# Kernel tuning notes

Hardware: AMD Instinct MI355X
Metric: run time of the kernel (lower is better)

Reference implementation:

```python
import jax, jax.numpy as jnp
import numpy as np

H, N, L = 512, 64, 2048


def setup_inputs() -> dict:
    key = jax.random.key(0)
    ks = jax.random.split(key, 9)
    x = jax.random.normal(ks[0], (L, H), jnp.float32)
    # HiPPO-style diagonal-plus-low-rank init (stable: Re(Lambda) < 0)
    lambda_re = -0.5 * jnp.ones((N,), jnp.float32)
    lambda_im = jnp.pi * jnp.arange(N, dtype=jnp.float32)
    p_re = jax.random.normal(ks[1], (N,), jnp.float32) / np.sqrt(2 * N)
    p_im = jax.random.normal(ks[2], (N,), jnp.float32) / np.sqrt(2 * N)
    b_re = jax.random.normal(ks[3], (N,), jnp.float32)
    b_im = jax.random.normal(ks[4], (N,), jnp.float32)
    c_re = jax.random.normal(ks[5], (N,), jnp.float32)
    c_im = jax.random.normal(ks[6], (N,), jnp.float32)
    log_step = jnp.array(np.log(0.01), jnp.float32)
    w1 = jax.random.normal(ks[7], (H, H), jnp.float32) / np.sqrt(H)
    bias1 = jnp.zeros((H,), jnp.float32)
    w2 = jax.random.normal(ks[8], (H, H), jnp.float32) / np.sqrt(H)
    bias2 = jnp.zeros((H,), jnp.float32)
    return dict(x=x, lambda_re=lambda_re, lambda_im=lambda_im, p_re=p_re, p_im=p_im,
                b_re=b_re, b_im=b_im, c_re=c_re, c_im=c_im, log_step=log_step,
                w1=w1, bias1=bias1, w2=w2, bias2=bias2)


def _discrete_dplr(Lam, P, B, C, step, seq_len):
    # Bilinear discretization of the DPLR SSM A = diag(Lam) - P P^* (annotated-S4).
    n = Lam.shape[0]
    I = jnp.eye(n, dtype=jnp.complex64)
    A = jnp.diag(Lam) - P[:, None] * jnp.conj(P)[None, :]
    A0 = (2.0 / step) * I + A
    Dd = jnp.diag(1.0 / (2.0 / step - Lam))  # (2/dt - Lam)^{-1} diagonal
    Qc = jnp.conj(P)[None, :]                 # (1, N)
    P2 = P[:, None]                           # (N, 1)
    A1 = Dd - (Dd @ P2) @ (Qc @ Dd) / (1.0 + (Qc @ Dd @ P2))  # Woodbury
    Ab = A1 @ A0                               # (N, N) discrete transition
    Bb = 2.0 * (A1 @ B[:, None])[:, 0]         # (N,)
    Cb = jnp.conj(
        C[None, :] @ jnp.conj(jnp.linalg.inv(I - jnp.linalg.matrix_power(Ab, seq_len)))
    )[0]                                       # (N,)
    return Ab, Bb, Cb


def reference(x, lambda_re, lambda_im, p_re, p_im, b_re, b_im, c_re, c_im,
              log_step, w1, bias1, w2, bias2):
    seq_len, hidden = x.shape
    Lam = (lambda_re + 1j * lambda_im).astype(jnp.complex64)
    P = (p_re + 1j * p_im).astype(jnp.complex64)
    B = (b_re + 1j * b_im).astype(jnp.complex64)
    C = (c_re + 1j * c_im).astype(jnp.complex64)
    step = jnp.exp(log_step)
    Ab, Bb, Cb = _discrete_dplr(Lam, P, B, C, step, seq_len)

    skip = x
    state0 = jnp.zeros((hidden, Lam.shape[0]), jnp.complex64)  # (H, N)

    def step_fn(state, u_l):  # u_l: (H,) real inputs at one timestep
        state = state @ Ab.T + u_l[:, None] * Bb[None, :]  # (H, N)
        y = (state @ Cb).real                               # (H,)
        return state, y

    _, ys = jax.lax.scan(step_fn, state0, x)  # ys: (L, H)
    h = jax.nn.gelu(ys)
    out = (h @ w1.T + bias1) * jax.nn.sigmoid(h @ w2.T + bias2)
    return skip + out
```

## Files before the change

### kernel.cpp

```cpp
#include <hip/hip_runtime.h>
#include <hip/hip_bf16.h>

typedef unsigned short u16;
typedef short s16x8 __attribute__((ext_vector_type(8)));
typedef u16 u16x8 __attribute__((ext_vector_type(8)));
typedef unsigned int u32x4 __attribute__((ext_vector_type(4)));
typedef float f32x4 __attribute__((ext_vector_type(4)));

struct cplx { float x, y; };

#define L_SEQ 2048
#define HID 512
#define NST 64

__device__ __align__(16) cplx g_khat[L_SEQ];
__device__ __align__(16) float g_k[L_SEQ];
__device__ __align__(16) u16 g_Td[32 * 64 * 64];
__device__ __align__(16) u16 g_Xt[HID * L_SEQ];
__device__ __align__(16) u16 g_W1[HID * HID];
__device__ __align__(16) u16 g_W2[HID * HID];
__device__ __align__(16) u16 g_H[L_SEQ * HID];

__device__ __forceinline__ u16 f2bf(float f) {
    union { __hip_bfloat16 h; u16 u; } cv;
    cv.h = __float2bfloat16(f);
    return cv.u;
}

__global__ __launch_bounds__(256) void fused_convert(
    const float* x, const float* w1, const float* w2,
    const float* lre, const float* lim, const float* pre, const float* pim,
    const float* bre, const float* bim, const float* cre, const float* cim,
    const float* lstep) {
    __shared__ float tile[64][65];
    __shared__ float sLre[NST], sLim[NST], sPre[NST], sPim[NST];
    __shared__ float sBre[NST], sBim[NST], sCre[NST], sCim[NST];
    int b = blockIdx.x, tid = threadIdx.x;
    if (b < 256) {
        int lt = b >> 3, ht = b & 7;
#pragma unroll
        for (int i = 0; i < 4; i++) {
            int idx = i * 256 + tid;
            int r = idx >> 4, c4 = idx & 15;
            f32x4 v = *(const f32x4*)&x[(lt * 64 + r) * HID + ht * 64 + c4 * 4];
            tile[r][c4 * 4 + 0] = v.x;
            tile[r][c4 * 4 + 1] = v.y;
            tile[r][c4 * 4 + 2] = v.z;
            tile[r][c4 * 4 + 3] = v.w;
        }
        __syncthreads();
#pragma unroll
        for (int i = 0; i < 2; i++) {
            int idx = i * 256 + tid;
            int rr = idx >> 3, c8 = idx & 7;
            u16x8 v;
#pragma unroll
            for (int q = 0; q < 8; q++) v[q] = f2bf(tile[c8 * 8 + q][rr]);
            *(u16x8*)&g_Xt[(ht * 64 + rr) * L_SEQ + lt * 64 + c8 * 8] = v;
        }
    } else if (b < 768) {
        int t = (b - 256) * 256 + tid;
        const float* src = (t < 65536) ? w1 : w2;
        u16* dst = (t < 65536) ? g_W1 : g_W2;
        int idx = (t < 65536) ? t : (t - 65536);
        float4 v = ((const float4*)src)[idx];
        unsigned long long pk = (unsigned long long)f2bf(v.x) |
                                ((unsigned long long)f2bf(v.y) << 16) |
                                ((unsigned long long)f2bf(v.z) << 32) |
                                ((unsigned long long)f2bf(v.w) << 48);
        ((unsigned long long*)dst)[idx] = pk;
    } else {
        if (tid < NST) {
            sLre[tid] = lre[tid]; sLim[tid] = lim[tid];
            sPre[tid] = pre[tid]; sPim[tid] = pim[tid];
            sBre[tid] = bre[tid]; sBim[tid] = bim[tid];
            sCre[tid] = cre[tid]; sCim[tid] = cim[tid];
        }
        __syncthreads();
        int j = (b - 768) * 256 + tid;
        float tdt = 2.0f * __expf(-lstep[0]);
        float th = 0.00306796157577128245f * j;
        float sn, cs;
        __sincosf(th, &sn, &cs);
        float aRe = tdt * (1.f - cs), aIm = tdt * sn;
        float bRe = 1.f + cs, bIm = -sn;
        float cBx = 0.f, cBy = 0.f, cPx = 0.f, cPy = 0.f;
        float pBx = 0.f, pBy = 0.f, pPx = 0.f, pPy = 0.f;
#pragma unroll 8
        for (int n = 0; n < NST; n++) {
            float Lre = sLre[n], Lim = sLim[n];
            float Dre = aRe - (bRe * Lre - bIm * Lim);
            float Dim = aIm - (bRe * Lim + bIm * Lre);
            float inv = 1.f / (Dre * Dre + Dim * Dim);
            float eRe = Dre * inv, eIm = -Dim * inv;
            float cRe = sCre[n], cIm = -sCim[n];
            float t1Re = cRe * eRe - cIm * eIm, t1Im = cRe * eIm + cIm * eRe;
            float qRe = sPre[n], qIm = -sPim[n];
            float t2Re = qRe * eRe - qIm * eIm, t2Im = qRe * eIm + qIm * eRe;
            float BRe = sBre[n], BIm = sBim[n], PRe = sPre[n], PIm = sPim[n];
            cBx += t1Re * BRe - t1Im * BIm; cBy += t1Re * BIm + t1Im * BRe;
            cPx += t1Re * PRe - t1Im * PIm; cPy += t1Re * PIm + t1Im * PRe;
            pBx += t2Re * BRe - t2Im * BIm; pBy += t2Re * BIm + t2Im * BRe;
            pPx += t2Re * PRe - t2Im * PIm; pPy += t2Re * PIm + t2Im * PRe;
        }
        float denx = 1.f + (bRe * pPx - bIm * pPy);
        float deny = (bRe * pPy + bIm * pPx);
        float bcPx = bRe * cPx - bIm * cPy;
        float bcPy = bRe * cPy + bIm * cPx;
        float numx = bcPx * pBx - bcPy * pBy;
        float numy = bcPx * pBy + bcPy * pBx;
        float dinv = 1.f / (denx * denx + deny * deny);
        float corx = (numx * denx + numy * deny) * dinv;
        float cory = (numy * denx - numx * deny) * dinv;
        g_khat[j] = { 2.f * (cBx - corx), 2.f * (cBy - cory) };
    }
}

__global__ __launch_bounds__(256) void k_ifft() {
    int tid = threadIdx.x;
    int l = tid & 63;
    int t = blockIdx.x * 4 + (tid >> 6);
    float acc = 0.f;
#pragma unroll
    for (int i = 0; i < 16; i++) {
        int j = l + 64 * i;
        cplx a = g_khat[j];
        cplx b = g_khat[(2048 - j) & 2047];
        float re = 0.5f * (a.x + b.x);
        float im = 0.5f * (a.y - b.y);
        int idx = (j * t) & 2047;
        float s, c;
        __sincosf(0.00306796157577128245f * idx, &s, &c);
        float wgt = (j == 0) ? 1.f : 2.f;
        acc += wgt * (re * c - im * s);
    }
    if (l == 0) acc += (1 - 2 * (t & 1)) * g_khat[1024].x;
#pragma unroll
    for (int off = 1; off < 64; off <<= 1) acc += __shfl_xor(acc, off);
    if (l == 0) g_k[t] = acc * (1.f / 2048.f);
}

__global__ __launch_bounds__(256) void build_Td() {
    int gid = blockIdx.x * 256 + threadIdx.x;
    int o = gid * 8;
    int d = o >> 12, rem = o & 4095;
    int r = rem >> 6, c0 = rem & 63;
    int base = d * 64 + r - c0;
    u16x8 v;
#pragma unroll
    for (int q = 0; q < 8; q++) {
        int idx = base - q;
        v[q] = (idx >= 0) ? f2bf(g_k[idx]) : (u16)0;
    }
    *(u16x8*)&g_Td[o] = v;
}

__global__ __launch_bounds__(256) void conv_gemm() {
    __shared__ __align__(16) u16 As[64 * 128];
    __shared__ __align__(16) u16 Bs[64 * 128];
    int tid = threadIdx.x, l = tid & 63, w = tid >> 6;
    int wm = w >> 1, wn = w & 1;
    int bm = blockIdx.x >> 3, bn = blockIdx.x & 7;
    f32x4 acc[2][2] = {};
    int nst = (bm >> 1) + 1;
    int row0 = tid >> 3, kc0 = tid & 7;
    int row1 = row0 + 32;
    int st00 = row0 * 16 + ((kc0) ^ (row0 & 7));
    int st01 = row0 * 16 + ((8 + kc0) ^ (row0 & 7));
    int st10 = row1 * 16 + ((kc0) ^ (row1 & 7));
    int st11 = row1 * 16 + ((8 + kc0) ^ (row1 & 7));
    const u32x4 zz = { 0, 0, 0, 0 };

#define LOADA(D00, D10, D01, D11, S)                                         \
    {                                                                        \
        int d0_ = bm - 2 * (S), d1_ = d0_ - 1;                               \
        if (d0_ >= 0) {                                                      \
            D00 = *(const u32x4*)&g_Td[d0_ * 4096 + row0 * 64 + kc0 * 8];    \
            D10 = *(const u32x4*)&g_Td[d0_ * 4096 + row1 * 64 + kc0 * 8];    \
        } else { D00 = zz; D10 = zz; }                                       \
        if (d1_ >= 0) {                                                      \
            D01 = *(const u32x4*)&g_Td[d1_ * 4096 + row0 * 64 + kc0 * 8];    \
            D11 = *(const u32x4*)&g_Td[d1_ * 4096 + row1 * 64 + kc0 * 8];    \
        } else { D01 = zz; D11 = zz; }                                       \
    }
#define LOADB(D00, D10, D01, D11, S)                                         \
    {                                                                        \
        int k0_ = (S) * 128;                                                 \
        D00 = *(const u32x4*)&g_Xt[(bn * 64 + row0) * L_SEQ + k0_ + kc0 * 8];        \
        D10 = *(const u32x4*)&g_Xt[(bn * 64 + row1) * L_SEQ + k0_ + kc0 * 8];        \
        D01 = *(const u32x4*)&g_Xt[(bn * 64 + row0) * L_SEQ + k0_ + 64 + kc0 * 8];   \
        D11 = *(const u32x4*)&g_Xt[(bn * 64 + row1) * L_SEQ + k0_ + 64 + kc0 * 8];   \
    }

#define CONV_COMPUTE                                                         \
    _Pragma("unroll")                                                        \
    for (int ks = 0; ks < 4; ks++) {                                         \
        s16x8 af[2], bf[2];                                                  \
        _Pragma("unroll")                                                    \
        for (int m = 0; m < 2; m++) {                                        \
            int row = wm * 32 + m * 16 + (l & 15);                           \
            int ch = (ks * 4 + (l >> 4)) ^ (row & 7);                        \
            af[m] = *(const s16x8*)&As[row * 128 + ch * 8];                  \
        }                                                                    \
        _Pragma("unroll")                                                    \
        for (int n = 0; n < 2; n++) {                                        \
            int col = wn * 32 + n * 16 + (l & 15);                           \
            int ch = (ks * 4 + (l >> 4)) ^ (col & 7);                        \
            bf[n] = *(const s16x8*)&Bs[col * 128 + ch * 8];                  \
        }                                                                    \
        _Pragma("unroll")                                                    \
        for (int m = 0; m < 2; m++)                                          \
            _Pragma("unroll")                                                \
            for (int n = 0; n < 2; n++)                                      \
                acc[m][n] = __builtin_amdgcn_mfma_f32_16x16x32_bf16(         \
                    af[m], bf[n], acc[m][n], 0, 0, 0);                       \
    }

#define CONV_STEP(A00, A10, A01, A11, B00, B10, B01, B11)                    \
    {                                                                        \
        __syncthreads();                                                     \
        ((u32x4*)As)[st00] = A00; ((u32x4*)As)[st10] = A10;                  \
        ((u32x4*)As)[st01] = A01; ((u32x4*)As)[st11] = A11;                  \
        ((u32x4*)Bs)[st00] = B00; ((u32x4*)Bs)[st10] = B10;                  \
        ((u32x4*)Bs)[st01] = B01; ((u32x4*)Bs)[st11] = B11;                  \
        if (s + 2 < nst) {                                                   \
            LOADA(A00, A10, A01, A11, s + 2);                                \
            LOADB(B00, B10, B01, B11, s + 2);                                \
        }                                                                    \
        __syncthreads();                                                     \
        CONV_COMPUTE;                                                        \
        s++;                                                                 \
    }

    u32x4 aA00, aA10, aA01, aA11, bA00, bA10, bA01, bA11;
    u32x4 aB00, aB10, aB01, aB11, bB00, bB10, bB01, bB11;
    LOADA(aA00, aA10, aA01, aA11, 0);
    LOADB(bA00, bA10, bA01, bA11, 0);
    int sp = (nst > 1) ? 1 : 0;
    LOADA(aB00, aB10, aB01, aB11, sp);
    LOADB(bB00, bB10, bB01, bB11, sp);
    int s = 0;
    while (true) {
        CONV_STEP(aA00, aA10, aA01, aA11, bA00, bA10, bA01, bA11);
        if (s >= nst) break;
        CONV_STEP(aB00, aB10, aB01, aB11, bB00, bB10, bB01, bB11);
        if (s >= nst) break;
    }
#undef CONV_STEP
#undef CONV_COMPUTE
#undef LOADA
#undef LOADB
#pragma unroll
    for (int m = 0; m < 2; m++)
#pragma unroll
        for (int n = 0; n < 2; n++)
#pragma unroll
            for (int r4 = 0; r4 < 4; r4++) {
                int row = bm * 64 + wm * 32 + m * 16 + (l >> 4) * 4 + r4;
                int col = bn * 64 + wn * 32 + n * 16 + (l & 15);
                float y = acc[m][n][r4];
                float u = 1.5957691216057308f * (y + 0.044715f * y * y * y);
                float th = 1.f - 2.f / (__expf(u) + 1.f);
                g_H[row * HID + col] = f2bf(0.5f * y * (1.f + th));
            }
}

__global__ __launch_bounds__(256) void ffn_gemm(const float* x, const float* b1,
                                                const float* b2, float* out) {
    __shared__ __align__(16) u16 As[64 * 128];
    __shared__ __align__(16) u16 B1s[64 * 128];
    __shared__ __align__(16) u16 B2s[64 * 128];
    int tid = threadIdx.x, l = tid & 63, w = tid >> 6;
    int wm = w >> 1, wn = w & 1;
    int bm = blockIdx.x >> 3, bn = blockIdx.x & 7;
    f32x4 acc1[2][2] = {}, acc2[2][2] = {};
    int row0 = tid >> 3, kc0 = tid & 7;
    int row1 = row0 + 32;
    int st00 = row0 * 16 + ((kc0) ^ (row0 & 7));
    int st01 = row0 * 16 + ((8 + kc0) ^ (row0 & 7));
    int st10 = row1 * 16 + ((kc0) ^ (row1 & 7));
    int st11 = row1 * 16 + ((8 + kc0) ^ (row1 & 7));
    const u16* aB = &g_H[(bm * 64) * HID];
    const u16* w1B = &g_W1[(bn * 64) * HID];
    const u16* w2B = &g_W2[(bn * 64) * HID];

#define LD3(DA0, DA1, DA2, DA3, D10, D11, D12, D13, D20, D21, D22, D23, S)   \
    {                                                                        \
        int k0_ = (S) * 128;                                                 \
        DA0 = *(const u32x4*)&aB[row0 * HID + k0_ + kc0 * 8];                \
        DA1 = *(const u32x4*)&aB[row1 * HID + k0_ + kc0 * 8];                \
        DA2 = *(const u32x4*)&aB[row0 * HID + k0_ + 64 + kc0 * 8];           \
        DA3 = *(const u32x4*)&aB[row1 * HID + k0_ + 64 + kc0 * 8];           \
        D10 = *(const u32x4*)&w1B[row0 * HID + k0_ + kc0 * 8];               \
        D11 = *(const u32x4*)&w1B[row1 * HID + k0_ + kc0 * 8];               \
        D12 = *(const u32x4*)&w1B[row0 * HID + k0_ + 64 + kc0 * 8];          \
        D13 = *(const u32x4*)&w1B[row1 * HID + k0_ + 64 + kc0 * 8];          \
        D20 = *(const u32x4*)&w2B[row0 * HID + k0_ + kc0 * 8];               \
        D21 = *(const u32x4*)&w2B[row1 * HID + k0_ + kc0 * 8];               \
        D22 = *(const u32x4*)&w2B[row0 * HID + k0_ + 64 + kc0 * 8];          \
        D23 = *(const u32x4*)&w2B[row1 * HID + k0_ + 64 + kc0 * 8];          \
    }

#define FFN_COMPUTE                                                          \
    _Pragma("unroll")                                                        \
    for (int ks = 0; ks < 4; ks++) {                                         \
        s16x8 af[2], b1f[2], b2f[2];                                         \
        _Pragma("unroll")                                                    \
        for (int m = 0; m < 2; m++) {                                        \
            int row = wm * 32 + m * 16 + (l & 15);                           \
            int ch = (ks * 4 + (l >> 4)) ^ (row & 7);                        \
            af[m] = *(const s16x8*)&As[row * 128 + ch * 8];                  \
        }                                                                    \
        _Pragma("unroll")                                                    \
        for (int n = 0; n < 2; n++) {                                        \
            int col = wn * 32 + n * 16 + (l & 15);                           \
            int ch = (ks * 4 + (l >> 4)) ^ (col & 7);                        \
            b1f[n] = *(const s16x8*)&B1s[col * 128 + ch * 8];                \
            b2f[n] = *(const s16x8*)&B2s[col * 128 + ch * 8];                \
        }                                                                    \
        _Pragma("unroll")                                                    \
        for (int m = 0; m < 2; m++)                                          \
            _Pragma("unroll")                                                \
            for (int n = 0; n < 2; n++) {                                    \
                acc1[m][n] = __builtin_amdgcn_mfma_f32_16x16x32_bf16(        \
                    af[m], b1f[n], acc1[m][n], 0, 0, 0);                     \
                acc2[m][n] = __builtin_amdgcn_mfma_f32_16x16x32_bf16(        \
                    af[m], b2f[n], acc2[m][n], 0, 0, 0);                     \
            }                                                                \
    }

#define FFN_STEP(SA0, SA1, SA2, SA3, S10, S11, S12, S13, S20, S21, S22, S23, SNEXT, DOPRE) \
    {                                                                        \
        __syncthreads();                                                     \
        ((u32x4*)As)[st00] = SA0;  ((u32x4*)As)[st10] = SA1;                 \
        ((u32x4*)As)[st01] = SA2;  ((u32x4*)As)[st11] = SA3;                 \
        ((u32x4*)B1s)[st00] = S10; ((u32x4*)B1s)[st10] = S11;                \
        ((u32x4*)B1s)[st01] = S12; ((u32x4*)B1s)[st11] = S13;                \
        ((u32x4*)B2s)[st00] = S20; ((u32x4*)B2s)[st10] = S21;                \
        ((u32x4*)B2s)[st01] = S22; ((u32x4*)B2s)[st11] = S23;                \
        if (DOPRE) LD3(SA0, SA1, SA2, SA3, S10, S11, S12, S13, S20, S21, S22, S23, SNEXT); \
        __syncthreads();                                                     \
        FFN_COMPUTE;                                                         \
    }

    u32x4 xA0, xA1, xA2, xA3, p10, p11, p12, p13, p20, p21, p22, p23;
    u32x4 yA0, yA1, yA2, yA3, q10, q11, q12, q13, q20, q21, q22, q23;
    LD3(xA0, xA1, xA2, xA3, p10, p11, p12, p13, p20, p21, p22, p23, 0);
    LD3(yA0, yA1, yA2, yA3, q10, q11, q12, q13, q20, q21, q22, q23, 1);
    FFN_STEP(xA0, xA1, xA2, xA3, p10, p11, p12, p13, p20, p21, p22, p23, 2, 1);
    FFN_STEP(yA0, yA1, yA2, yA3, q10, q11, q12, q13, q20, q21, q22, q23, 3, 1);
    FFN_STEP(xA0, xA1, xA2, xA3, p10, p11, p12, p13, p20, p21, p22, p23, 0, 0);
    FFN_STEP(yA0, yA1, yA2, yA3, q10, q11, q12, q13, q20, q21, q22, q23, 0, 0);
#undef FFN_STEP
#undef FFN_COMPUTE
#undef LD3
#pragma unroll
    for (int m = 0; m < 2; m++)
#pragma unroll
        for (int n = 0; n < 2; n++)
#pragma unroll
            for (int r4 = 0; r4 < 4; r4++) {
                int row = bm * 64 + wm * 32 + m * 16 + (l >> 4) * 4 + r4;
                int col = bn * 64 + wn * 32 + n * 16 + (l & 15);
                float g1 = acc1[m][n][r4] + b1[col];
                float g2 = acc2[m][n][r4] + b2[col];
                float sg = 1.f / (1.f + __expf(-g2));
                out[row * HID + col] = x[row * HID + col] + g1 * sg;
            }
}

extern "C" void kernel_launch(void* const* d_in, const int* in_sizes, int n_in,
                              void* d_out, int out_size, void* d_ws, size_t ws_size,
                              hipStream_t stream) {
    const float* x = (const float*)d_in[0];
    const float* lre = (const float*)d_in[1];
    const float* lim = (const float*)d_in[2];
    const float* pre = (const float*)d_in[3];
    const float* pim = (const float*)d_in[4];
    const float* bre = (const float*)d_in[5];
    const float* bim = (const float*)d_in[6];
    const float* cre = (const float*)d_in[7];
    const float* cim = (const float*)d_in[8];
    const float* lstep = (const float*)d_in[9];
    const float* w1 = (const float*)d_in[10];
    const float* b1 = (const float*)d_in[11];
    const float* w2 = (const float*)d_in[12];
    const float* b2 = (const float*)d_in[13];
    float* out = (float*)d_out;

    fused_convert<<<776, 256, 0, stream>>>(x, w1, w2, lre, lim, pre, pim,
                                           bre, bim, cre, cim, lstep);
    k_ifft<<<512, 256, 0, stream>>>();
    build_Td<<<64, 256, 0, stream>>>();
    conv_gemm<<<256, 256, 0, stream>>>();
    ffn_gemm<<<256, 256, 0, stream>>>(x, b1, b2, out);
}
```

Baseline: 48.80 us.

## Fuse five launches into one persistent kernel with grid-wide atomic barriers

Merges the convert, iFFT, Toeplitz build, conv GEMM and FFN GEMM kernels into a single 256-block persistent kernel. Stages are separated by software grid barriers built from atomic counters in workspace, which is zeroed by a memset before each launch. The aim is to remove the launch gaps and tail effects between the five small kernels. In exchange it depends on all 256 blocks being co-resident, and the spin-wait barriers plus shared-memory reuse could add stalls.

```diff
diff --git a/kernel.cpp b/kernel.cpp
--- a/kernel.cpp
+++ b/kernel.cpp
@@ -27,346 +27,370 @@
     return cv.u;
 }
 
-__global__ __launch_bounds__(256) void fused_convert(
+__global__ __launch_bounds__(256) void mega(
     const float* x, const float* w1, const float* w2,
     const float* lre, const float* lim, const float* pre, const float* pim,
     const float* bre, const float* bim, const float* cre, const float* cim,
-    const float* lstep) {
-    __shared__ float tile[64][65];
-    __shared__ float sLre[NST], sLim[NST], sPre[NST], sPim[NST];
-    __shared__ float sBre[NST], sBim[NST], sCre[NST], sCim[NST];
-    int b = blockIdx.x, tid = threadIdx.x;
-    if (b < 256) {
-        int lt = b >> 3, ht = b & 7;
-#pragma unroll
-        for (int i = 0; i < 4; i++) {
-            int idx = i * 256 + tid;
-            int r = idx >> 4, c4 = idx & 15;
-            f32x4 v = *(const f32x4*)&x[(lt * 64 + r) * HID + ht * 64 + c4 * 4];
-            tile[r][c4 * 4 + 0] = v.x;
-            tile[r][c4 * 4 + 1] = v.y;
-            tile[r][c4 * 4 + 2] = v.z;
-            tile[r][c4 * 4 + 3] = v.w;
-        }
-        __syncthreads();
-#pragma unroll
-        for (int i = 0; i < 2; i++) {
-            int idx = i * 256 + tid;
-            int rr = idx >> 3, c8 = idx & 7;
-            u16x8 v;
-#pragma unroll
-            for (int q = 0; q < 8; q++) v[q] = f2bf(tile[c8 * 8 + q][rr]);
-            *(u16x8*)&g_Xt[(ht * 64 + rr) * L_SEQ + lt * 64 + c8 * 8] = v;
-        }
-    } else if (b < 768) {
-        int t = (b - 256) * 256 + tid;
-        const float* src = (t < 65536) ? w1 : w2;
-        u16* dst = (t < 65536) ? g_W1 : g_W2;
-        int idx = (t < 65536) ? t : (t - 65536);
-        float4 v = ((const float4*)src)[idx];
-        unsigned long long pk = (unsigned long long)f2bf(v.x) |
-                                ((unsigned long long)f2bf(v.y) << 16) |
-                                ((unsigned long long)f2bf(v.z) << 32) |
-                                ((unsigned long long)f2bf(v.w) << 48);
-        ((unsigned long long*)dst)[idx] = pk;
-    } else {
-        if (tid < NST) {
-            sLre[tid] = lre[tid]; sLim[tid] = lim[tid];
-            sPre[tid] = pre[tid]; sPim[tid] = pim[tid];
-            sBre[tid] = bre[tid]; sBim[tid] = bim[tid];
-            sCre[tid] = cre[tid]; sCim[tid] = cim[tid];
-        }
-        __syncthreads();
-        int j = (b - 768) * 256 + tid;
-        float tdt = 2.0f * __expf(-lstep[0]);
-        float th = 0.00306796157577128245f * j;
-        float sn, cs;
-        __sincosf(th, &sn, &cs);
-        float aRe = tdt * (1.f - cs), aIm = tdt * sn;
-        float bRe = 1.f + cs, bIm = -sn;
-        float cBx = 0.f, cBy = 0.f, cPx = 0.f, cPy = 0.f;
-        float pBx = 0.f, pBy = 0.f, pPx = 0.f, pPy = 0.f;
-#pragma unroll 8
-        for (int n = 0; n < NST; n++) {
-            float Lre = sLre[n], Lim = sLim[n];
-            float Dre = aRe - (bRe * Lre - bIm * Lim);
-            float Dim = aIm - (bRe * Lim + bIm * Lre);
-            float inv = 1.f / (Dre * Dre + Dim * Dim);
-            float eRe = Dre * inv, eIm = -Dim * inv;
-            float cRe = sCre[n], cIm = -sCim[n];
-            float t1Re = cRe * eRe - cIm * eIm, t1Im = cRe * eIm + cIm * eRe;
-            float qRe = sPre[n], qIm = -sPim[n];
-            float t2Re = qRe * eRe - qIm * eIm, t2Im = qRe * eIm + qIm * eRe;
-            float BRe = sBre[n], BIm = sBim[n], PRe = sPre[n], PIm = sPim[n];
-            cBx += t1Re * BRe - t1Im * BIm; cBy += t1Re * BIm + t1Im * BRe;
-            cPx += t1Re * PRe - t1Im * PIm; cPy += t1Re * PIm + t1Im * PRe;
-            pBx += t2Re * BRe - t2Im * BIm; pBy += t2Re * BIm + t2Im * BRe;
-            pPx += t2Re * PRe - t2Im * PIm; pPy += t2Re * PIm + t2Im * PRe;
-        }
-        float denx = 1.f + (bRe * pPx - bIm * pPy);
-        float deny = (bRe * pPy + bIm * pPx);
-        float bcPx = bRe * cPx - bIm * cPy;
-        float bcPy = bRe * cPy + bIm * cPx;
-        float numx = bcPx * pBx - bcPy * pBy;
-        float numy = bcPx * pBy + bcPy * pBx;
-        float dinv = 1.f / (denx * denx + deny * deny);
-        float corx = (numx * denx + numy * deny) * dinv;
-        float cory = (numy * denx - numx * deny) * dinv;
-        g_khat[j] = { 2.f * (cBx - corx), 2.f * (cBy - cory) };
-    }
-}
-
-__global__ __launch_bounds__(256) void k_ifft() {
-    int tid = threadIdx.x;
-    int l = tid & 63;
-    int t = blockIdx.x * 4 + (tid >> 6);
-    float acc = 0.f;
-#pragma unroll
-    for (int i = 0; i < 16; i++) {
-        int j = l + 64 * i;
-        cplx a = g_khat[j];
-        cplx b = g_khat[(2048 - j) & 2047];
-        float re = 0.5f * (a.x + b.x);
-        float im = 0.5f * (a.y - b.y);
-        int idx = (j * t) & 2047;
-        float s, c;
-        __sincosf(0.00306796157577128245f * idx, &s, &c);
-        float wgt = (j == 0) ? 1.f : 2.f;
-        acc += wgt * (re * c - im * s);
-    }
-    if (l == 0) acc += (1 - 2 * (t & 1)) * g_khat[1024].x;
-#pragma unroll
-    for (int off = 1; off < 64; off <<= 1) acc += __shfl_xor(acc, off);
-    if (l == 0) g_k[t] = acc * (1.f / 2048.f);
-}
-
-__global__ __launch_bounds__(256) void build_Td() {
-    int gid = blockIdx.x * 256 + threadIdx.x;
-    int o = gid * 8;
-    int d = o >> 12, rem = o & 4095;
-    int r = rem >> 6, c0 = rem & 63;
-    int base = d * 64 + r - c0;
-    u16x8 v;
-#pragma unroll
-    for (int q = 0; q < 8; q++) {
-        int idx = base - q;
-        v[q] = (idx >= 0) ? f2bf(g_k[idx]) : (u16)0;
-    }
-    *(u16x8*)&g_Td[o] = v;
-}
-
-__global__ __launch_bounds__(256) void conv_gemm() {
-    __shared__ __align__(16) u16 As[64 * 128];
-    __shared__ __align__(16) u16 Bs[64 * 128];
-    int tid = threadIdx.x, l = tid & 63, w = tid >> 6;
-    int wm = w >> 1, wn = w & 1;
-    int bm = blockIdx.x >> 3, bn = blockIdx.x & 7;
-    f32x4 acc[2][2] = {};
-    int nst = (bm >> 1) + 1;
-    int row0 = tid >> 3, kc0 = tid & 7;
-    int row1 = row0 + 32;
-    int st00 = row0 * 16 + ((kc0) ^ (row0 & 7));
-    int st01 = row0 * 16 + ((8 + kc0) ^ (row0 & 7));
-    int st10 = row1 * 16 + ((kc0) ^ (row1 & 7));
-    int st11 = row1 * 16 + ((8 + kc0) ^ (row1 & 7));
-    const u32x4 zz = { 0, 0, 0, 0 };
-
-#define LOADA(D00, D10, D01, D11, S)                                         \
-    {                                                                        \
-        int d0_ = bm - 2 * (S), d1_ = d0_ - 1;                               \
-        if (d0_ >= 0) {                                                      \
-            D00 = *(const u32x4*)&g_Td[d0_ * 4096 + row0 * 64 + kc0 * 8];    \
-            D10 = *(const u32x4*)&g_Td[d0_ * 4096 + row1 * 64 + kc0 * 8];    \
-        } else { D00 = zz; D10 = zz; }                                       \
-        if (d1_ >= 0) {                                                      \
-            D01 = *(const u32x4*)&g_Td[d1_ * 4096 + row0 * 64 + kc0 * 8];    \
-            D11 = *(const u32x4*)&g_Td[d1_ * 4096 + row1 * 64 + kc0 * 8];    \
-        } else { D01 = zz; D11 = zz; }                                       \
-    }
-#define LOADB(D00, D10, D01, D11, S)                                         \
-    {                                                                        \
-        int k0_ = (S) * 128;                                                 \
-        D00 = *(const u32x4*)&g_Xt[(bn * 64 + row0) * L_SEQ + k0_ + kc0 * 8];        \
-        D10 = *(const u32x4*)&g_Xt[(bn * 64 + row1) * L_SEQ + k0_ + kc0 * 8];        \
-        D01 = *(const u32x4*)&g_Xt[(bn * 64 + row0) * L_SEQ + k0_ + 64 + kc0 * 8];   \
-        D11 = *(const u32x4*)&g_Xt[(bn * 64 + row1) * L_SEQ + k0_ + 64 + kc0 * 8];   \
-    }
-
-#define CONV_COMPUTE                                                         \
-    _Pragma("unroll")                                                        \
-    for (int ks = 0; ks < 4; ks++) {                                         \
-        s16x8 af[2], bf[2];                                                  \
-        _Pragma("unroll")                                                    \
-        for (int m = 0; m < 2; m++) {                                        \
-            int row = wm * 32 + m * 16 + (l & 15);                           \
-            int ch = (ks * 4 + (l >> 4)) ^ (row & 7);                        \
-            af[m] = *(const s16x8*)&As[row * 128 + ch * 8];                  \
-        }                                                                    \
-        _Pragma("unroll")                                                    \
-        for (int n = 0; n < 2; n++) {                                        \
-            int col = wn * 32 + n * 16 + (l & 15);                           \
-            int ch = (ks * 4 + (l >> 4)) ^ (col & 7);                        \
-            bf[n] = *(const s16x8*)&Bs[col * 128 + ch * 8];                  \
-        }                                                                    \
-        _Pragma("unroll")                                                    \
-        for (int m = 0; m < 2; m++)                                          \
-            _Pragma("unroll")                                                \
-            for (int n = 0; n < 2; n++)                                      \
-                acc[m][n] = __builtin_amdgcn_mfma_f32_16x16x32_bf16(         \
-                    af[m], bf[n], acc[m][n], 0, 0, 0);                       \
-    }
-
-#define CONV_STEP(A00, A10, A01, A11, B00, B10, B01, B11)                    \
+    const float* lstep, const float* b1, const float* b2, float* out,
+    unsigned* bar) {
+    __shared__ __align__(16) char smem[49152];
+    int bid = blockIdx.x, tid = threadIdx.x;
+
+#define GBAR(I)                                                              \
     {                                                                        \
         __syncthreads();                                                     \
-        ((u32x4*)As)[st00] = A00; ((u32x4*)As)[st10] = A10;                  \
-        ((u32x4*)As)[st01] = A01; ((u32x4*)As)[st11] = A11;                  \
-        ((u32x4*)Bs)[st00] = B00; ((u32x4*)Bs)[st10] = B10;                  \
-        ((u32x4*)Bs)[st01] = B01; ((u32x4*)Bs)[st11] = B11;                  \
-        if (s + 2 < nst) {                                                   \
-            LOADA(A00, A10, A01, A11, s + 2);                                \
-            LOADB(B00, B10, B01, B11, s + 2);                                \
+        if (tid == 0) {                                                      \
+            __threadfence();                                                 \
+            atomicAdd(&bar[I], 1u);                                          \
+            while (atomicAdd(&bar[I], 0u) < 256u) { __builtin_amdgcn_s_sleep(2); } \
+            __threadfence();                                                 \
         }                                                                    \
         __syncthreads();                                                     \
-        CONV_COMPUTE;                                                        \
-        s++;                                                                 \
-    }
-
-    u32x4 aA00, aA10, aA01, aA11, bA00, bA10, bA01, bA11;
-    u32x4 aB00, aB10, aB01, aB11, bB00, bB10, bB01, bB11;
-    LOADA(aA00, aA10, aA01, aA11, 0);
-    LOADB(bA00, bA10, bA01, bA11, 0);
-    int sp = (nst > 1) ? 1 : 0;
-    LOADA(aB00, aB10, aB01, aB11, sp);
-    LOADB(bB00, bB10, bB01, bB11, sp);
-    int s = 0;
-    while (true) {
-        CONV_STEP(aA00, aA10, aA01, aA11, bA00, bA10, bA01, bA11);
-        if (s >= nst) break;
-        CONV_STEP(aB00, aB10, aB01, aB11, bB00, bB10, bB01, bB11);
-        if (s >= nst) break;
-    }
+    }
+
+    for (int u = bid; u < 776; u += 256) {
+        if (u < 256) {
+            float (*tile)[65] = (float(*)[65])smem;
+            int lt = u >> 3, ht = u & 7;
+#pragma unroll
+            for (int i = 0; i < 4; i++) {
+                int idx = i * 256 + tid;
+                int r = idx >> 4, c4 = idx & 15;
+                f32x4 v = *(const f32x4*)&x[(lt * 64 + r) * HID + ht * 64 + c4 * 4];
+                tile[r][c4 * 4 + 0] = v.x;
+                tile[r][c4 * 4 + 1] = v.y;
+                tile[r][c4 * 4 + 2] = v.z;
+                tile[r][c4 * 4 + 3] = v.w;
+            }
+            __syncthreads();
+#pragma unroll
+            for (int i = 0; i < 2; i++) {
+                int idx = i * 256 + tid;
+                int rr = idx >> 3, c8 = idx & 7;
+                u16x8 v;
+#pragma unroll
+                for (int q = 0; q < 8; q++) v[q] = f2bf(tile[c8 * 8 + q][rr]);
+                *(u16x8*)&g_Xt[(ht * 64 + rr) * L_SEQ + lt * 64 + c8 * 8] = v;
+            }
+        } else if (u < 768) {
+            int t = (u - 256) * 256 + tid;
+            const float* src = (t < 65536) ? w1 : w2;
+            u16* dst = (t < 65536) ? g_W1 : g_W2;
+            int idx = (t < 65536) ? t : (t - 65536);
+            float4 v = ((const float4*)src)[idx];
+            unsigned long long pk = (unsigned long long)f2bf(v.x) |
+                                    ((unsigned long long)f2bf(v.y) << 16) |
+                                    ((unsigned long long)f2bf(v.z) << 32) |
+                                    ((unsigned long long)f2bf(v.w) << 48);
+            ((unsigned long long*)dst)[idx] = pk;
+        } else {
+            float* sLre = (float*)(smem + 16640);
+            float* sLim = sLre + 64;
+            float* sPre = sLim + 64;
+            float* sPim = sPre + 64;
+            float* sBre = sPim + 64;
+            float* sBim = sBre + 64;
+            float* sCre = sBim + 64;
+            float* sCim = sCre + 64;
+            if (tid < NST) {
+                sLre[tid] = lre[tid]; sLim[tid] = lim[tid];
+                sPre[tid] = pre[tid]; sPim[tid] = pim[tid];
+                sBre[tid] = bre[tid]; sBim[tid] = bim[tid];
+                sCre[tid] = cre[tid]; sCim[tid] = cim[tid];
+            }
+            __syncthreads();
+            int j = (u - 768) * 256 + tid;
+            float tdt = 2.0f * __expf(-lstep[0]);
+            float th = 0.00306796157577128245f * j;
+            float sn, cs;
+            __sincosf(th, &sn, &cs);
+            float aRe = tdt * (1.f - cs), aIm = tdt * sn;
+            float bRe = 1.f + cs, bIm = -sn;
+            float cBx = 0.f, cBy = 0.f, cPx = 0.f, cPy = 0.f;
+            float pBx = 0.f, pBy = 0.f, pPx = 0.f, pPy = 0.f;
+#pragma unroll 8
+            for (int n = 0; n < NST; n++) {
+                float Lre = sLre[n], Lim = sLim[n];
+                float Dre = aRe - (bRe * Lre - bIm * Lim);
+                float Dim = aIm - (bRe * Lim + bIm * Lre);
+                float inv = 1.f / (Dre * Dre + Dim * Dim);
+                float eRe = Dre * inv, eIm = -Dim * inv;
+                float cRe = sCre[n], cIm = -sCim[n];
+                float t1Re = cRe * eRe - cIm * eIm, t1Im = cRe * eIm + cIm * eRe;
+                float qRe = sPre[n], qIm = -sPim[n];
+                float t2Re = qRe * eRe - qIm * eIm, t2Im = qRe * eIm + qIm * eRe;
+                float BRe = sBre[n], BIm = sBim[n], PRe = sPre[n], PIm = sPim[n];
+                cBx += t1Re * BRe - t1Im * BIm; cBy += t1Re * BIm + t1Im * BRe;
+                cPx += t1Re * PRe - t1Im * PIm; cPy += t1Re * PIm + t1Im * PRe;
+                pBx += t2Re * BRe - t2Im * BIm; pBy += t2Re * BIm + t2Im * BRe;
+                pPx += t2Re * PRe - t2Im * PIm; pPy += t2Re * PIm + t2Im * PRe;
+            }
+            float denx = 1.f + (bRe * pPx - bIm * pPy);
+            float deny = (bRe * pPy + bIm * pPx);
+            float bcPx = bRe * cPx - bIm * cPy;
+            float bcPy = bRe * cPy + bIm * cPx;
+            float numx = bcPx * pBx - bcPy * pBy;
+            float numy = bcPx * pBy + bcPy * pBx;
+            float dinv = 1.f / (denx * denx + deny * deny);
+            float corx = (numx * denx + numy * deny) * dinv;
+            float cory = (numy * denx - numx * deny) * dinv;
+            g_khat[j] = { 2.f * (cBx - corx), 2.f * (cBy - cory) };
+        }
+    }
+    GBAR(0);
+
+    for (int u = bid; u < 512; u += 256) {
+        int l = tid & 63;
+        int t = u * 4 + (tid >> 6);
+        float acc = 0.f;
+#pragma unroll
+        for (int i = 0; i < 16; i++) {
+            int j = l + 64 * i;
+            cplx a = g_khat[j];
+            cplx b = g_khat[(2048 - j) & 2047];
+            float re = 0.5f * (a.x + b.x);
+            float im = 0.5f * (a.y - b.y);
+            int idx = (j * t) & 2047;
+            float s, c;
+            __sincosf(0.00306796157577128245f * idx, &s, &c);
+            float wgt = (j == 0) ? 1.f : 2.f;
+            acc += wgt * (re * c - im * s);
+        }
+        if (l == 0) acc += (1 - 2 * (t & 1)) * g_khat[1024].x;
+#pragma unroll
+        for (int off = 1; off < 64; off <<= 1) acc += __shfl_xor(acc, off);
+        if (l == 0) g_k[t] = acc * (1.f / 2048.f);
+    }
+    GBAR(1);
+
+    {
+        int unit = bid * 256 + tid;
+        if (unit < 16384) {
+            int o = unit * 8;
+            int d = o >> 12, rem = o & 4095;
+            int r = rem >> 6, c0 = rem & 63;
+            int base = d * 64 + r - c0;
+            u16x8 v;
+#pragma unroll
+            for (int q = 0; q < 8; q++) {
+                int idx = base - q;
+                v[q] = (idx >= 0) ? f2bf(g_k[idx]) : (u16)0;
+            }
+            *(u16x8*)&g_Td[o] = v;
+        }
+    }
+    GBAR(2);
+
+    {
+        u16* As = (u16*)smem;
+        u16* Bs = (u16*)(smem + 16384);
+        int l = tid & 63, w = tid >> 6;
+        int wm = w >> 1, wn = w & 1;
+        int bm = bid >> 3, bn = bid & 7;
+        f32x4 acc[2][2] = {};
+        int nst = (bm >> 1) + 1;
+        int row0 = tid >> 3, kc0 = tid & 7;
+        int row1 = row0 + 32;
+        int st00 = row0 * 16 + ((kc0) ^ (row0 & 7));
+        int st01 = row0 * 16 + ((8 + kc0) ^ (row0 & 7));
+        int st10 = row1 * 16 + ((kc0) ^ (row1 & 7));
+        int st11 = row1 * 16 + ((8 + kc0) ^ (row1 & 7));
+        const u32x4 zz = { 0, 0, 0, 0 };
+
+#define LOADA(D00, D10, D01, D11, S)                                         \
+        {                                                                    \
+            int d0_ = bm - 2 * (S), d1_ = d0_ - 1;                           \
+            if (d0_ >= 0) {                                                  \
+                D00 = *(const u32x4*)&g_Td[d0_ * 4096 + row0 * 64 + kc0 * 8];\
+                D10 = *(const u32x4*)&g_Td[d0_ * 4096 + row1 * 64 + kc0 * 8];\
+            } else { D00 = zz; D10 = zz; }                                   \
+            if (d1_ >= 0) {                                                  \
+                D01 = *(const u32x4*)&g_Td[d1_ * 4096 + row0 * 64 + kc0 * 8];\
+                D11 = *(const u32x4*)&g_Td[d1_ * 4096 + row1 * 64 + kc0 * 8];\
+            } else { D01 = zz; D11 = zz; }                                   \
+        }
+#define LOADB(D00, D10, D01, D11, S)                                         \
+        {                                                                    \
+            int k0_ = (S) * 128;                                             \
+            D00 = *(const u32x4*)&g_Xt[(bn * 64 + row0) * L_SEQ + k0_ + kc0 * 8];      \
+            D10 = *(const u32x4*)&g_Xt[(bn * 64 + row1) * L_SEQ + k0_ + kc0 * 8];      \
+            D01 = *(const u32x4*)&g_Xt[(bn * 64 + row0) * L_SEQ + k0_ + 64 + kc0 * 8]; \
+            D11 = *(const u32x4*)&g_Xt[(bn * 64 + row1) * L_SEQ + k0_ + 64 + kc0 * 8]; \
+        }
+#define CONV_COMPUTE                                                         \
+        _Pragma("unroll")                                                    \
+        for (int ks = 0; ks < 4; ks++) {                                     \
+            s16x8 af[2], bf[2];                                              \
+            _Pragma("unroll")                                                \
+            for (int m = 0; m < 2; m++) {                                    \
+                int row = wm * 32 + m * 16 + (l & 15);                       \
+                int ch = (ks * 4 + (l >> 4)) ^ (row & 7);                    \
+                af[m] = *(const s16x8*)&As[row * 128 + ch * 8];              \
+            }                                                                \
+            _Pragma("unroll")                                                \
+            for (int n = 0; n < 2; n++) {                                    \
+                int col = wn * 32 + n * 16 + (l & 15);                       \
+                int ch = (ks * 4 + (l >> 4)) ^ (col & 7);                    \
+                bf[n] = *(const s16x8*)&Bs[col * 128 + ch * 8];              \
+            }                                                                \
+            _Pragma("unroll")                                                \
+            for (int m = 0; m < 2; m++)                                      \
+                _Pragma("unroll")                                            \
+                for (int n = 0; n < 2; n++)                                  \
+                    acc[m][n] = __builtin_amdgcn_mfma_f32_16x16x32_bf16(     \
+                        af[m], bf[n], acc[m][n], 0, 0, 0);                   \
+        }
+#define CONV_STEP(A00, A10, A01, A11, B00, B10, B01, B11)                    \
+        {                                                                    \
+            __syncthreads();                                                 \
+            ((u32x4*)As)[st00] = A00; ((u32x4*)As)[st10] = A10;              \
+            ((u32x4*)As)[st01] = A01; ((u32x4*)As)[st11] = A11;              \
+            ((u32x4*)Bs)[st00] = B00; ((u32x4*)Bs)[st10] = B10;              \
+            ((u32x4*)Bs)[st01] = B01; ((u32x4*)Bs)[st11] = B11;              \
+            if (s + 2 < nst) {                                               \
+                LOADA(A00, A10, A01, A11, s + 2);                            \
+                LOADB(B00, B10, B01, B11, s + 2);                            \
+            }                                                                \
+            __syncthreads();                                                 \
+            CONV_COMPUTE;                                                    \
+            s++;                                                             \
+        }
+
+        u32x4 aA00, aA10, aA01, aA11, bA00, bA10, bA01, bA11;
+        u32x4 aB00, aB10, aB01, aB11, bB00, bB10, bB01, bB11;
+        LOADA(aA00, aA10, aA01, aA11, 0);
+        LOADB(bA00, bA10, bA01, bA11, 0);
+        int sp = (nst > 1) ? 1 : 0;
+        LOADA(aB00, aB10, aB01, aB11, sp);
+        LOADB(bB00, bB10, bB01, bB11, sp);
+        int s = 0;
+        while (true) {
+            CONV_STEP(aA00, aA10, aA01, aA11, bA00, bA10, bA01, bA11);
+            if (s >= nst) break;
+            CONV_STEP(aB00, aB10, aB01, aB11, bB00, bB10, bB01, bB11);
+            if (s >= nst) break;
+        }
 #undef CONV_STEP
 #undef CONV_COMPUTE
 #undef LOADA
 #undef LOADB
 #pragma unroll
-    for (int m = 0; m < 2; m++)
-#pragma unroll
-        for (int n = 0; n < 2; n++)
-#pragma unroll
-            for (int r4 = 0; r4 < 4; r4++) {
-                int row = bm * 64 + wm * 32 + m * 16 + (l >> 4) * 4 + r4;
-                int col = bn * 64 + wn * 32 + n * 16 + (l & 15);
-                float y = acc[m][n][r4];
-                float u = 1.5957691216057308f * (y + 0.044715f * y * y * y);
-                float th = 1.f - 2.f / (__expf(u) + 1.f);
-                g_H[row * HID + col] = f2bf(0.5f * y * (1.f + th));
-            }
-}
-
-__global__ __launch_bounds__(256) void ffn_gemm(const float* x, const float* b1,
-                                                const float* b2, float* out) {
-    __shared__ __align__(16) u16 As[64 * 128];
-    __shared__ __align__(16) u16 B1s[64 * 128];
-    __shared__ __align__(16) u16 B2s[64 * 128];
-    int tid = threadIdx.x, l = tid & 63, w = tid >> 6;
-    int wm = w >> 1, wn = w & 1;
-    int bm = blockIdx.x >> 3, bn = blockIdx.x & 7;
-    f32x4 acc1[2][2] = {}, acc2[2][2] = {};
-    int row0 = tid >> 3, kc0 = tid & 7;
-    int row1 = row0 + 32;
-    int st00 = row0 * 16 + ((kc0) ^ (row0 & 7));
-    int st01 = row0 * 16 + ((8 + kc0) ^ (row0 & 7));
-    int st10 = row1 * 16 + ((kc0) ^ (row1 & 7));
-    int st11 = row1 * 16 + ((8 + kc0) ^ (row1 & 7));
-    const u16* aB = &g_H[(bm * 64) * HID];
-    const u16* w1B = &g_W1[(bn * 64) * HID];
-    const u16* w2B = &g_W2[(bn * 64) * HID];
+        for (int m = 0; m < 2; m++)
+#pragma unroll
+            for (int n = 0; n < 2; n++)
+#pragma unroll
+                for (int r4 = 0; r4 < 4; r4++) {
+                    int row = bm * 64 + wm * 32 + m * 16 + (l >> 4) * 4 + r4;
+                    int col = bn * 64 + wn * 32 + n * 16 + (l & 15);
+                    float y = acc[m][n][r4];
+                    float uu = 1.5957691216057308f * (y + 0.044715f * y * y * y);
+                    float th = 1.f - 2.f / (__expf(uu) + 1.f);
+                    g_H[row * HID + col] = f2bf(0.5f * y * (1.f + th));
+                }
+    }
+    GBAR(3);
+
+    {
+        u16* As = (u16*)smem;
+        u16* B1s = (u16*)(smem + 16384);
+        u16* B2s = (u16*)(smem + 32768);
+        int l = tid & 63, w = tid >> 6;
+        int wm = w >> 1, wn = w & 1;
+        int bm = bid >> 3, bn = bid & 7;
+        f32x4 acc1[2][2] = {}, acc2[2][2] = {};
+        int row0 = tid >> 3, kc0 = tid & 7;
+        int row1 = row0 + 32;
+        int st00 = row0 * 16 + ((kc0) ^ (row0 & 7));
+        int st01 = row0 * 16 + ((8 + kc0) ^ (row0 & 7));
+        int st10 = row1 * 16 + ((kc0) ^ (row1 & 7));
+        int st11 = row1 * 16 + ((8 + kc0) ^ (row1 & 7));
+        const u16* aB = &g_H[(bm * 64) * HID];
+        const u16* w1B = &g_W1[(bn * 64) * HID];
+        const u16* w2B = &g_W2[(bn * 64) * HID];
 
 #define LD3(DA0, DA1, DA2, DA3, D10, D11, D12, D13, D20, D21, D22, D23, S)   \
-    {                                                                        \
-        int k0_ = (S) * 128;                                                 \
-        DA0 = *(const u32x4*)&aB[row0 * HID + k0_ + kc0 * 8];                \
-        DA1 = *(const u32x4*)&aB[row1 * HID + k0_ + kc0 * 8];                \
-        DA2 = *(const u32x4*)&aB[row0 * HID + k0_ + 64 + kc0 * 8];           \
-        DA3 = *(const u32x4*)&aB[row1 * HID + k0_ + 64 + kc0 * 8];           \
-        D10 = *(const u32x4*)&w1B[row0 * HID + k0_ + kc0 * 8];               \
-        D11 = *(const u32x4*)&w1B[row1 * HID + k0_ + kc0 * 8];               \
-        D12 = *(const u32x4*)&w1B[row0 * HID + k0_ + 64 + kc0 * 8];          \
-        D13 = *(const u32x4*)&w1B[row1 * HID + k0_ + 64 + kc0 * 8];          \
-        D20 = *(const u32x4*)&w2B[row0 * HID + k0_ + kc0 * 8];               \
-        D21 = *(const u32x4*)&w2B[row1 * HID + k0_ + kc0 * 8];               \
-        D22 = *(const u32x4*)&w2B[row0 * HID + k0_ + 64 + kc0 * 8];          \
-        D23 = *(const u32x4*)&w2B[row1 * HID + k0_ + 64 + kc0 * 8];          \
-    }
-
+        {                                                                    \
+            int k0_ = (S) * 128;                                             \
+            DA0 = *(const u32x4*)&aB[row0 * HID + k0_ + kc0 * 8];            \
+            DA1 = *(const u32x4*)&aB[row1 * HID + k0_ + kc0 * 8];            \
+            DA2 = *(const u32x4*)&aB[row0 * HID + k0_ + 64 + kc0 * 8];       \
+            DA3 = *(const u32x4*)&aB[row1 * HID + k0_ + 64 + kc0 * 8];       \
+            D10 = *(const u32x4*)&w1B[row0 * HID + k0_ + kc0 * 8];           \
+            D11 = *(const u32x4*)&w1B[row1 * HID + k0_ + kc0 * 8];           \
+            D12 = *(const u32x4*)&w1B[row0 * HID + k0_ + 64 + kc0 * 8];      \
+            D13 = *(const u32x4*)&w1B[row1 * HID + k0_ + 64 + kc0 * 8];      \
+            D20 = *(const u32x4*)&w2B[row0 * HID + k0_ + kc0 * 8];           \
+            D21 = *(const u32x4*)&w2B[row1 * HID + k0_ + kc0 * 8];           \
+            D22 = *(const u32x4*)&w2B[row0 * HID + k0_ + 64 + kc0 * 8];      \
+            D23 = *(const u32x4*)&w2B[row1 * HID + k0_ + 64 + kc0 * 8];      \
+        }
 #define FFN_COMPUTE                                                          \
-    _Pragma("unroll")                                                        \
-    for (int ks = 0; ks < 4; ks++) {                                         \
-        s16x8 af[2], b1f[2], b2f[2];                                         \
         _Pragma("unroll")                                                    \
-        for (int m = 0; m < 2; m++) {                                        \
-            int row = wm * 32 + m * 16 + (l & 15);                           \
-            int ch = (ks * 4 + (l >> 4)) ^ (row & 7);                        \
-            af[m] = *(const s16x8*)&As[row * 128 + ch * 8];                  \
-        }                                                                    \
-        _Pragma("unroll")                                                    \
-        for (int n = 0; n < 2; n++) {                                        \
-            int col = wn * 32 + n * 16 + (l & 15);                           \
-            int ch = (ks * 4 + (l >> 4)) ^ (col & 7);                        \
-            b1f[n] = *(const s16x8*)&B1s[col * 128 + ch * 8];                \
-            b2f[n] = *(const s16x8*)&B2s[col * 128 + ch * 8];                \
-        }                                                                    \
-        _Pragma("unroll")                                                    \
-        for (int m = 0; m < 2; m++)                                          \
+        for (int ks = 0; ks < 4; ks++) {                                     \
+            s16x8 af[2], b1f[2], b2f[2];                                     \
+            _Pragma("unroll")                                                \
+            for (int m = 0; m < 2; m++) {                                    \
+                int row = wm * 32 + m * 16 + (l & 15);                       \
+                int ch = (ks * 4 + (l >> 4)) ^ (row & 7);                    \
+                af[m] = *(const s16x8*)&As[row * 128 + ch * 8];              \
+            }                                                                \
             _Pragma("unroll")                                                \
             for (int n = 0; n < 2; n++) {                                    \
-                acc1[m][n] = __builtin_amdgcn_mfma_f32_16x16x32_bf16(        \
-                    af[m], b1f[n], acc1[m][n], 0, 0, 0);                     \
-                acc2[m][n] = __builtin_amdgcn_mfma_f32_16x16x32_bf16(        \
-                    af[m], b2f[n], acc2[m][n], 0, 0, 0);                     \
+                int col = wn * 32 + n * 16 + (l & 15);                       \
+                int ch = (ks * 4 + (l >> 4)) ^ (col & 7);                    \
+                b1f[n] = *(const s16x8*)&B1s[col * 128 + ch * 8];            \
+                b2f[n] = *(const s16x8*)&B2s[col * 128 + ch * 8];            \
             }                                                                \
-    }
-
+            _Pragma("unroll")                                                \
+            for (int m = 0; m < 2; m++)                                      \
+                _Pragma("unroll")                                            \
+                for (int n = 0; n < 2; n++) {                                \
+                    acc1[m][n] = __builtin_amdgcn_mfma_f32_16x16x32_bf16(    \
+                        af[m], b1f[n], acc1[m][n], 0, 0, 0);                 \
+                    acc2[m][n] = __builtin_amdgcn_mfma_f32_16x16x32_bf16(    \
+                        af[m], b2f[n], acc2[m][n], 0, 0, 0);                 \
+                }                                                            \
+        }
 #define FFN_STEP(SA0, SA1, SA2, SA3, S10, S11, S12, S13, S20, S21, S22, S23, SNEXT, DOPRE) \
-    {                                                                        \
-        __syncthreads();                                                     \
-        ((u32x4*)As)[st00] = SA0;  ((u32x4*)As)[st10] = SA1;                 \
-        ((u32x4*)As)[st01] = SA2;  ((u32x4*)As)[st11] = SA3;                 \
-        ((u32x4*)B1s)[st00] = S10; ((u32x4*)B1s)[st10] = S11;                \
-        ((u32x4*)B1s)[st01] = S12; ((u32x4*)B1s)[st11] = S13;                \
-        ((u32x4*)B2s)[st00] = S20; ((u32x4*)B2s)[st10] = S21;                \
-        ((u32x4*)B2s)[st01] = S22; ((u32x4*)B2s)[st11] = S23;                \
-        if (DOPRE) LD3(SA0, SA1, SA2, SA3, S10, S11, S12, S13, S20, S21, S22, S23, SNEXT); \
-        __syncthreads();                                                     \
-        FFN_COMPUTE;                                                         \
-    }
-
-    u32x4 xA0, xA1, xA2, xA3, p10, p11, p12, p13, p20, p21, p22, p23;
-    u32x4 yA0, yA1, yA2, yA3, q10, q11, q12, q13, q20, q21, q22, q23;
-    LD3(xA0, xA1, xA2, xA3, p10, p11, p12, p13, p20, p21, p22, p23, 0);
-    LD3(yA0, yA1, yA2, yA3, q10, q11, q12, q13, q20, q21, q22, q23, 1);
-    FFN_STEP(xA0, xA1, xA2, xA3, p10, p11, p12, p13, p20, p21, p22, p23, 2, 1);
-    FFN_STEP(yA0, yA1, yA2, yA3, q10, q11, q12, q13, q20, q21, q22, q23, 3, 1);
-    FFN_STEP(xA0, xA1, xA2, xA3, p10, p11, p12, p13, p20, p21, p22, p23, 0, 0);
-    FFN_STEP(yA0, yA1, yA2, yA3, q10, q11, q12, q13, q20, q21, q22, q23, 0, 0);
+        {                                                                    \
+            __syncthreads();                                                 \
+            ((u32x4*)As)[st00] = SA0;  ((u32x4*)As)[st10] = SA1;             \
+            ((u32x4*)As)[st01] = SA2;  ((u32x4*)As)[st11] = SA3;             \
+            ((u32x4*)B1s)[st00] = S10; ((u32x4*)B1s)[st10] = S11;            \
+            ((u32x4*)B1s)[st01] = S12; ((u32x4*)B1s)[st11] = S13;            \
+            ((u32x4*)B2s)[st00] = S20; ((u32x4*)B2s)[st10] = S21;            \
+            ((u32x4*)B2s)[st01] = S22; ((u32x4*)B2s)[st11] = S23;            \
+            if (DOPRE) LD3(SA0, SA1, SA2, SA3, S10, S11, S12, S13, S20, S21, S22, S23, SNEXT); \
+            __syncthreads();                                                 \
+            FFN_COMPUTE;                                                     \
+        }
+
+        u32x4 xA0, xA1, xA2, xA3, p10, p11, p12, p13, p20, p21, p22, p23;
+        u32x4 yA0, yA1, yA2, yA3, q10, q11, q12, q13, q20, q21, q22, q23;
+        LD3(xA0, xA1, xA2, xA3, p10, p11, p12, p13, p20, p21, p22, p23, 0);
+        LD3(yA0, yA1, yA2, yA3, q10, q11, q12, q13, q20, q21, q22, q23, 1);
+        FFN_STEP(xA0, xA1, xA2, xA3, p10, p11, p12, p13, p20, p21, p22, p23, 2, 1);
+        FFN_STEP(yA0, yA1, yA2, yA3, q10, q11, q12, q13, q20, q21, q22, q23, 3, 1);
+        FFN_STEP(xA0, xA1, xA2, xA3, p10, p11, p12, p13, p20, p21, p22, p23, 0, 0);
+        FFN_STEP(yA0, yA1, yA2, yA3, q10, q11, q12, q13, q20, q21, q22, q23, 0, 0);
 #undef FFN_STEP
 #undef FFN_COMPUTE
 #undef LD3
 #pragma unroll
-    for (int m = 0; m < 2; m++)
-#pragma unroll
-        for (int n = 0; n < 2; n++)
-#pragma unroll
-            for (int r4 = 0; r4 < 4; r4++) {
-                int row = bm * 64 + wm * 32 + m * 16 + (l >> 4) * 4 + r4;
-                int col = bn * 64 + wn * 32 + n * 16 + (l & 15);
-                float g1 = acc1[m][n][r4] + b1[col];
-                float g2 = acc2[m][n][r4] + b2[col];
-                float sg = 1.f / (1.f + __expf(-g2));
-                out[row * HID + col] = x[row * HID + col] + g1 * sg;
-            }
+        for (int m = 0; m < 2; m++)
+#pragma unroll
+            for (int n = 0; n < 2; n++)
+#pragma unroll
+                for (int r4 = 0; r4 < 4; r4++) {
+                    int row = bm * 64 + wm * 32 + m * 16 + (l >> 4) * 4 + r4;
+                    int col = bn * 64 + wn * 32 + n * 16 + (l & 15);
+                    float g1 = acc1[m][n][r4] + b1[col];
+                    float g2 = acc2[m][n][r4] + b2[col];
+                    float sg = 1.f / (1.f + __expf(-g2));
+                    out[row * HID + col] = x[row * HID + col] + g1 * sg;
+                }
+    }
+#undef GBAR
 }
 
 extern "C" void kernel_launch(void* const* d_in, const int* in_sizes, int n_in,
@@ -387,11 +411,9 @@
     const float* w2 = (const float*)d_in[12];
     const float* b2 = (const float*)d_in[13];
     float* out = (float*)d_out;
-
-    fused_convert<<<776, 256, 0, stream>>>(x, w1, w2, lre, lim, pre, pim,
-                                           bre, bim, cre, cim, lstep);
-    k_ifft<<<512, 256, 0, stream>>>();
-    build_Td<<<64, 256, 0, stream>>>();
-    conv_gemm<<<256, 256, 0, stream>>>();
-    ffn_gemm<<<256, 256, 0, stream>>>(x, b1, b2, out);
+    unsigned* bar = (unsigned*)d_ws;
+
+    hipMemsetAsync(d_ws, 0, 64, stream);
+    mega<<<256, 256, 0, stream>>>(x, w1, w2, lre, lim, pre, pim, bre, bim,
+                                  cre, cim, lstep, b1, b2, out, bar);
 }
```

Result: slower. 121.9 us (+149.8%).
